# Optimization experiments

Measured on AMD Instinct MI355X. Metric: run time of the kernel, lower is better.

Reference implementation:

```python
import jax, jax.numpy as jnp
import numpy as np

# Representative causal-LM config (pre-LN GPT/Llama-style, eager attention)
L, D, H, FF, V = 2, 2048, 16, 8192, 32000
B, S = 2, 1024
DH = D // H
NEG = -1e9


def setup_inputs() -> dict:
    key = jax.random.key(0)
    ks = jax.random.split(key, 10)
    p = lambda k, shape: jax.random.normal(k, shape, dtype=jnp.float32) * 0.02
    return {
        "input_ids": jax.random.randint(ks[0], (B, S), 0, V),
        "attention_mask": jnp.ones((B, S), dtype=jnp.int32),
        "emb": p(ks[1], (V, D)),
        "ln1_g": jnp.ones((L, D)), "ln1_b": jnp.zeros((L, D)),
        "Wqkv": p(ks[2], (L, D, 3 * D)),
        "Wo": p(ks[3], (L, D, D)),
        "ln2_g": jnp.ones((L, D)), "ln2_b": jnp.zeros((L, D)),
        "W1": p(ks[4], (L, D, FF)), "W2": p(ks[5], (L, FF, D)),
        "lnf_g": jnp.ones((D,)), "lnf_b": jnp.zeros((D,)),
        "Wc1": p(ks[6], (D, D)), "bc1": jnp.zeros((D,)),
        "Wc2": p(ks[7], (D, 2)), "bc2": jnp.zeros((2,)),
    }


def _ln(x, g, b):
    m = x.mean(-1, keepdims=True)
    v = ((x - m) ** 2).mean(-1, keepdims=True)
    return (x - m) * jax.lax.rsqrt(v + 1e-5) * g + b


def _transformer_reward(input_ids, attention_mask, emb, ln1_g, ln1_b, Wqkv, Wo,
                        ln2_g, ln2_b, W1, W2, lnf_g, lnf_b, Wc1, bc1, Wc2, bc2):
    x = emb[input_ids]                                  # [B,S,D] embedding lookup
    causal = jnp.tril(jnp.ones((S, S), dtype=bool))     # [S,S]
    pad = attention_mask.astype(bool)[:, None, None, :] # [B,1,1,S]
    bias = jnp.where(causal[None, None] & pad, 0.0, NEG).astype(jnp.float32)
    scale = 1.0 / np.sqrt(DH).astype(np.float32)
    for l in range(L):
        h = _ln(x, ln1_g[l], ln1_b[l])
        qkv = h @ Wqkv[l]                               # [B,S,3D]
        q, k, v = jnp.split(qkv, 3, axis=-1)
        q = q.reshape(B, S, H, DH).transpose(0, 2, 1, 3)
        k = k.reshape(B, S, H, DH).transpose(0, 2, 1, 3)
        v = v.reshape(B, S, H, DH).transpose(0, 2, 1, 3)
        # eager attention: full [B,H,S,S] score matrix (as in attn_implementation='eager')
        scores = jnp.einsum('bhqd,bhkd->bhqk', q, k) * scale + bias
        attn = jax.nn.softmax(scores, axis=-1)
        o = jnp.einsum('bhqk,bhkd->bhqd', attn, v).transpose(0, 2, 1, 3).reshape(B, S, D)
        x = x + o @ Wo[l]
        h = _ln(x, ln2_g[l], ln2_b[l])
        x = x + jax.nn.gelu(h @ W1[l]) @ W2[l]
    hs = _ln(x, lnf_g, lnf_b)                           # hidden_states[-1]
    m = attention_mask[:, :, None].astype(jnp.float32)
    mean = (hs * m).sum(axis=1) / jnp.clip(m.sum(axis=1), 1e-9)  # masked mean pool
    logits = jnp.tanh(mean @ Wc1 + bc1) @ Wc2 + bc2     # classifier head
    return jax.nn.softmax(logits, axis=-1)[:, 1]        # rewards [B]


def reference(input_ids, attention_mask, emb, ln1_g, ln1_b, Wqkv, Wo,
              ln2_g, ln2_b, W1, W2, lnf_g, lnf_b, Wc1, bc1, Wc2, bc2):
    return _transformer_reward(input_ids, attention_mask, emb, ln1_g, ln1_b, Wqkv, Wo,
                               ln2_g, ln2_b, W1, W2, lnf_g, lnf_b, Wc1, bc1, Wc2, bc2)
```

## Files before the change

kernel.cpp:

```cpp
#include <hip/hip_runtime.h>
#include <hip/hip_bf16.h>

using bf16 = __hip_bfloat16;
typedef short s16x8 __attribute__((ext_vector_type(8)));
typedef float f32x4 __attribute__((ext_vector_type(4)));

static constexpr int D  = 2048;
static constexpr int H  = 16;
static constexpr int FF = 8192;
static constexpr int S  = 1024;
static constexpr int NB = 2;
static constexpr int DH = 128;
static constexpr int L  = 2;
static constexpr int BS = NB * S;
static constexpr int BH = NB * H;
static constexpr int D3 = 3 * D;

__device__ __forceinline__ float wave_sum(float v) {
#pragma unroll
  for (int o = 32; o > 0; o >>= 1) v += __shfl_down(v, o, 64);
  return v;
}
__device__ __forceinline__ float wave_max(float v) {
#pragma unroll
  for (int o = 32; o > 0; o >>= 1) v = fmaxf(v, __shfl_down(v, o, 64));
  return v;
}

__device__ __forceinline__ void gll16(const void* g, void* l) {
  __builtin_amdgcn_global_load_lds(
      (const __attribute__((address_space(1))) unsigned int*)g,
      (__attribute__((address_space(3))) unsigned int*)l, 16, 0, 0);
}

__device__ __forceinline__ float gelu_tanh(float x) {
  return 0.5f * x * (1.0f + tanhf(0.7978845608028654f * (x + 0.044715f * x * x * x)));
}

__device__ __forceinline__ void stv(float* p, long i, float v) { p[i] = v; }
__device__ __forceinline__ void stv(bf16* p, long i, float v)  { p[i] = __float2bfloat16(v); }

template <int EPI>
__launch_bounds__(256)
__global__ void gemm_k(const bf16* __restrict__ A, int lda, long sAb, long sAh,
                       const bf16* __restrict__ Bt, int ldb, long sBb, long sBh,
                       void* __restrict__ Cp, int ldc, long sCb, long sCh,
                       const float* __restrict__ resid, int K, int nH) {
  __shared__ __align__(16) bf16 lsA[2][128 * 32];
  __shared__ __align__(16) bf16 lsB[2][128 * 32];
  const int tid = threadIdx.x;
  const int zb = blockIdx.z / nH, zh = blockIdx.z % nH;
  const int m0 = blockIdx.y * 128, n0 = blockIdx.x * 128;
  const int sr = tid >> 2, sc = (tid & 3) * 8;
  const bf16* Ag = A + zb * sAb + zh * sAh + (long)(m0 + sr) * lda + sc;
  const bf16* Bg = Bt + zb * sBb + zh * sBh + (long)(n0 + sr) * ldb + sc;
  const long a64 = 64L * lda, b64 = 64L * ldb;

  const int lane = tid & 63, wv = tid >> 6;
  const int wm = (wv >> 1) * 64, wn = (wv & 1) * 64;
  const int fl = lane & 15, fg = lane >> 4;

  f32x4 acc[4][4];
#pragma unroll
  for (int i = 0; i < 4; i++)
#pragma unroll
    for (int j = 0; j < 4; j++) acc[i][j] = (f32x4){0.f, 0.f, 0.f, 0.f};

  gll16(Ag, lsA[0] + tid * 8);
  gll16(Ag + a64, lsA[0] + 2048 + tid * 8);
  gll16(Bg, lsB[0] + tid * 8);
  gll16(Bg + b64, lsB[0] + 2048 + tid * 8);
  __syncthreads();

  int it = 0;
  for (int k0 = 0; k0 < K; k0 += 32, it ^= 1) {
    const int nxt = it ^ 1;
    if (k0 + 32 < K) {
      gll16(Ag + k0 + 32, lsA[nxt] + tid * 8);
      gll16(Ag + a64 + k0 + 32, lsA[nxt] + 2048 + tid * 8);
      gll16(Bg + k0 + 32, lsB[nxt] + tid * 8);
      gll16(Bg + b64 + k0 + 32, lsB[nxt] + 2048 + tid * 8);
    }
    s16x8 af[4], bq[4];
#pragma unroll
    for (int i = 0; i < 4; i++) {
      af[i] = *(const s16x8*)(lsA[it] + (wm + i * 16 + fl) * 32 + fg * 8);
      bq[i] = *(const s16x8*)(lsB[it] + (wn + i * 16 + fl) * 32 + fg * 8);
    }
#pragma unroll
    for (int i = 0; i < 4; i++)
#pragma unroll
      for (int j = 0; j < 4; j++)
        acc[i][j] = __builtin_amdgcn_mfma_f32_16x16x32_bf16(af[i], bq[j], acc[i][j], 0, 0, 0);
    __syncthreads();
  }

  const long offC = zb * sCb + zh * sCh;
#pragma unroll
  for (int i = 0; i < 4; i++) {
#pragma unroll
    for (int j = 0; j < 4; j++) {
      const int row = m0 + wm + i * 16 + fg * 4;
      const int col = n0 + wn + j * 16 + fl;
#pragma unroll
      for (int r = 0; r < 4; r++) {
        const long ci = offC + (long)(row + r) * ldc + col;
        float v = acc[i][j][r];
        if (EPI == 0) {
          ((float*)Cp)[ci] = v;
        } else if (EPI == 1) {
          ((bf16*)Cp)[ci] = __float2bfloat16(v);
        } else if (EPI == 2) {
          ((float*)Cp)[ci] = v + resid[ci];
        } else {
          ((bf16*)Cp)[ci] = __float2bfloat16(gelu_tanh(v));
        }
      }
    }
  }
}

__launch_bounds__(256)
__global__ void reduce4_k(const float* __restrict__ p, float* __restrict__ x) {
  const long i = (long)blockIdx.x * 256 + threadIdx.x;
  const long n = (long)BS * D / 4;
  const float4 a = ((const float4*)p)[i];
  const float4 b = ((const float4*)p)[i + n];
  const float4 c = ((const float4*)p)[i + 2 * n];
  const float4 d2 = ((const float4*)p)[i + 3 * n];
  float4 xv = ((float4*)x)[i];
  xv.x += a.x + b.x + c.x + d2.x;
  xv.y += a.y + b.y + c.y + d2.y;
  xv.z += a.z + b.z + c.z + d2.z;
  xv.w += a.w + b.w + c.w + d2.w;
  ((float4*)x)[i] = xv;
}

__launch_bounds__(256)
__global__ void transcast_k(const float* __restrict__ in, bf16* __restrict__ out,
                            int R, int C) {
  __shared__ float tile[32][33];
  const int tx = threadIdx.x, ty = threadIdx.y;
  const int c0 = blockIdx.x * 32, r0 = blockIdx.y * 32;
#pragma unroll
  for (int k = 0; k < 4; k++)
    tile[ty + 8 * k][tx] = in[(long)(r0 + ty + 8 * k) * C + c0 + tx];
  __syncthreads();
#pragma unroll
  for (int k = 0; k < 4; k++)
    out[(long)(c0 + ty + 8 * k) * R + r0 + tx] = __float2bfloat16(tile[tx][ty + 8 * k]);
}

__launch_bounds__(256)
__global__ void vtrans_k(const bf16* __restrict__ qkv, bf16* __restrict__ Vt) {
  __shared__ bf16 tile[32][33];
  const int z = blockIdx.z, b = z / H, h = z % H;
  const int d0 = blockIdx.x * 32, s0 = blockIdx.y * 32;
  const int tx = threadIdx.x, ty = threadIdx.y;
#pragma unroll
  for (int k = 0; k < 4; k++)
    tile[ty + 8 * k][tx] =
        qkv[(long)(b * S + s0 + ty + 8 * k) * D3 + 2 * D + h * DH + d0 + tx];
  __syncthreads();
#pragma unroll
  for (int k = 0; k < 4; k++)
    Vt[((long)z * DH + d0 + ty + 8 * k) * S + s0 + tx] = tile[tx][ty + 8 * k];
}

template <typename OutT>
__launch_bounds__(256)
__global__ void ln_k(const float* __restrict__ x, const float* __restrict__ g,
                     const float* __restrict__ bb, OutT* __restrict__ out) {
  __shared__ float sA[4], sB[4];
  const long row = blockIdx.x;
  const int tid = threadIdx.x;
  const float4* xr = (const float4*)(x + row * D);
  float4 v0 = xr[tid], v1 = xr[tid + 256];
  float s = v0.x + v0.y + v0.z + v0.w + v1.x + v1.y + v1.z + v1.w;
  float ss = v0.x * v0.x + v0.y * v0.y + v0.z * v0.z + v0.w * v0.w +
             v1.x * v1.x + v1.y * v1.y + v1.z * v1.z + v1.w * v1.w;
  s = wave_sum(s);
  ss = wave_sum(ss);
  const int lane = tid & 63, wv = tid >> 6;
  if (lane == 0) { sA[wv] = s; sB[wv] = ss; }
  __syncthreads();
  s = sA[0] + sA[1] + sA[2] + sA[3];
  ss = sB[0] + sB[1] + sB[2] + sB[3];
  const float mean = s * (1.f / D);
  const float var = ss * (1.f / D) - mean * mean;
  const float rstd = rsqrtf(var + 1e-5f);
  const float4* gv = (const float4*)g;
  const float4* bv = (const float4*)bb;
  float4 g0 = gv[tid], g1 = gv[tid + 256], c0 = bv[tid], c1 = bv[tid + 256];
  OutT* orow = out + row * D;
  stv(orow, 4 * tid + 0, (v0.x - mean) * rstd * g0.x + c0.x);
  stv(orow, 4 * tid + 1, (v0.y - mean) * rstd * g0.y + c0.y);
  stv(orow, 4 * tid + 2, (v0.z - mean) * rstd * g0.z + c0.z);
  stv(orow, 4 * tid + 3, (v0.w - mean) * rstd * g0.w + c0.w);
  stv(orow, 1024 + 4 * tid + 0, (v1.x - mean) * rstd * g1.x + c1.x);
  stv(orow, 1024 + 4 * tid + 1, (v1.y - mean) * rstd * g1.y + c1.y);
  stv(orow, 1024 + 4 * tid + 2, (v1.z - mean) * rstd * g1.z + c1.z);
  stv(orow, 1024 + 4 * tid + 3, (v1.w - mean) * rstd * g1.w + c1.w);
}

__launch_bounds__(256)
__global__ void embed_k(const int* __restrict__ ids, const float* __restrict__ emb,
                        float* __restrict__ x) {
  const long gid = (long)blockIdx.x * 256 + threadIdx.x;
  const int tok = (int)(gid >> 9);
  const int c = (int)(gid & 511);
  const int id = ids[tok];
  ((float4*)x)[gid] = ((const float4*)(emb + (long)id * D))[c];
}

__launch_bounds__(256)
__global__ void softmax_k(float* __restrict__ scores, const int* __restrict__ amask,
                          float scale) {
  __shared__ float sred[4];
  const int q = blockIdx.x, z = blockIdx.y, b = z / H;
  float* row = scores + ((long)z * S + q) * S;
  const int tid = threadIdx.x;
  const int lane = tid & 63, wv = tid >> 6;
  float v[4];
  float mx = -3.4e38f;
#pragma unroll
  for (int i = 0; i < 4; i++) {
    const int k = tid + i * 256;
    const float s = row[k] * scale;
    const bool ok = (k <= q) && (amask[b * S + k] != 0);
    v[i] = s + (ok ? 0.f : -1e9f);
    mx = fmaxf(mx, v[i]);
  }
  mx = wave_max(mx);
  if (lane == 0) sred[wv] = mx;
  __syncthreads();
  mx = fmaxf(fmaxf(sred[0], sred[1]), fmaxf(sred[2], sred[3]));
  __syncthreads();
  float e[4], sm = 0.f;
#pragma unroll
  for (int i = 0; i < 4; i++) {
    e[i] = __expf(v[i] - mx);
    sm += e[i];
  }
  sm = wave_sum(sm);
  if (lane == 0) sred[wv] = sm;
  __syncthreads();
  sm = sred[0] + sred[1] + sred[2] + sred[3];
  const float inv = 1.f / sm;
  bf16* orow = (bf16*)row;
#pragma unroll
  for (int i = 0; i < 4; i++) orow[tid + i * 256] = __float2bfloat16(e[i] * inv);
}

__launch_bounds__(256)
__global__ void pool_k(const float* __restrict__ hs, const int* __restrict__ amask,
                       float* __restrict__ pooled) {
  const int d = blockIdx.x * 256 + threadIdx.x;
  const int b = blockIdx.y;
  float s = 0.f, cnt = 0.f;
  for (int i = 0; i < S; i++) {
    const float m = (float)amask[b * S + i];
    s += hs[((long)(b * S + i)) * D + d] * m;
    cnt += m;
  }
  pooled[b * D + d] = s / fmaxf(cnt, 1e-9f);
}

__launch_bounds__(256)
__global__ void head1_k(const float* __restrict__ pooled, const float* __restrict__ Wc1,
                        const float* __restrict__ bc1, float* __restrict__ t) {
  const int j = blockIdx.x * 256 + threadIdx.x;
  const int b = blockIdx.y;
  float s = bc1[j];
  for (int d = 0; d < D; d++) s += pooled[b * D + d] * Wc1[(long)d * D + j];
  t[b * D + j] = tanhf(s);
}

__launch_bounds__(256)
__global__ void head2_k(const float* __restrict__ t, const float* __restrict__ Wc2,
                        const float* __restrict__ bc2, float* __restrict__ out) {
  __shared__ float red[4][4];
  const int tid = threadIdx.x;
  const int lane = tid & 63, wv = tid >> 6;
  float a[4] = {0.f, 0.f, 0.f, 0.f};
  for (int j = tid; j < D; j += 256) {
    const float w0 = Wc2[j * 2 + 0], w1 = Wc2[j * 2 + 1];
    const float t0 = t[j], t1 = t[D + j];
    a[0] += t0 * w0; a[1] += t0 * w1; a[2] += t1 * w0; a[3] += t1 * w1;
  }
#pragma unroll
  for (int c = 0; c < 4; c++) a[c] = wave_sum(a[c]);
  if (lane == 0) {
#pragma unroll
    for (int c = 0; c < 4; c++) red[wv][c] = a[c];
  }
  __syncthreads();
  if (tid == 0) {
    float tot[4];
#pragma unroll
    for (int c = 0; c < 4; c++) tot[c] = red[0][c] + red[1][c] + red[2][c] + red[3][c];
    const float l00 = tot[0] + bc2[0], l01 = tot[1] + bc2[1];
    const float l10 = tot[2] + bc2[0], l11 = tot[3] + bc2[1];
    out[0] = 1.f / (1.f + __expf(l00 - l01));
    out[1] = 1.f / (1.f + __expf(l10 - l11));
  }
}

extern "C" void kernel_launch(void* const* d_in, const int* in_sizes, int n_in,
                              void* d_out, int out_size, void* d_ws, size_t ws_size,
                              hipStream_t stream) {
  (void)in_sizes; (void)n_in; (void)out_size; (void)ws_size;
  const int*   ids   = (const int*)d_in[0];
  const int*   amask = (const int*)d_in[1];
  const float* emb   = (const float*)d_in[2];
  const float* ln1g  = (const float*)d_in[3];
  const float* ln1b  = (const float*)d_in[4];
  const float* Wqkv  = (const float*)d_in[5];
  const float* Wo    = (const float*)d_in[6];
  const float* ln2g  = (const float*)d_in[7];
  const float* ln2b  = (const float*)d_in[8];
  const float* W1    = (const float*)d_in[9];
  const float* W2    = (const float*)d_in[10];
  const float* lnfg  = (const float*)d_in[11];
  const float* lnfb  = (const float*)d_in[12];
  const float* Wc1   = (const float*)d_in[13];
  const float* bc1   = (const float*)d_in[14];
  const float* Wc2   = (const float*)d_in[15];
  const float* bc2   = (const float*)d_in[16];
  float* out = (float*)d_out;

  char* ws = (char*)d_ws;
  size_t off = 0;
  auto alloc = [&](size_t bytes) {
    size_t r = off;
    off += (bytes + 255) & ~(size_t)255;
    return r;
  };
  bf16* Wqkv_t = (bf16*)(ws + alloc((size_t)D3 * D * 2));
  bf16* Wo_t   = (bf16*)(ws + alloc((size_t)D * D * 2));
  bf16* W1_t   = (bf16*)(ws + alloc((size_t)FF * D * 2));
  bf16* W2_t   = (bf16*)(ws + alloc((size_t)D * FF * 2));
  float* x     = (float*)(ws + alloc((size_t)BS * D * 4));
  bf16* h      = (bf16*)(ws + alloc((size_t)BS * D * 2));
  bf16* qkv    = (bf16*)(ws + alloc((size_t)BS * D3 * 2));
  bf16* Vt     = (bf16*)(ws + alloc((size_t)BH * DH * S * 2));
  bf16* o_buf  = (bf16*)(ws + alloc((size_t)BS * D * 2));
  float* pooled= (float*)(ws + alloc((size_t)NB * D * 4));
  float* tb    = (float*)(ws + alloc((size_t)NB * D * 4));
  char* big    = ws + alloc((size_t)BH * S * S * 4);
  float* scores = (float*)big;
  bf16*  ffb    = (bf16*)big;
  float* hs     = (float*)big;
  float* parts  = (float*)(big + ((size_t)BS * FF * 2 + 255 & ~(size_t)255));

  const float scale = 0.088388347648318447f;
  dim3 blk(256);
  dim3 tblk(32, 8);

  embed_k<<<4096, blk, 0, stream>>>(ids, emb, x);

  for (int l = 0; l < L; l++) {
    transcast_k<<<dim3(D3 / 32, D / 32), tblk, 0, stream>>>(Wqkv + (size_t)l * D * D3, Wqkv_t, D, D3);
    transcast_k<<<dim3(D / 32, D / 32), tblk, 0, stream>>>(Wo + (size_t)l * D * D, Wo_t, D, D);
    transcast_k<<<dim3(FF / 32, D / 32), tblk, 0, stream>>>(W1 + (size_t)l * D * FF, W1_t, D, FF);
    transcast_k<<<dim3(D / 32, FF / 32), tblk, 0, stream>>>(W2 + (size_t)l * FF * D, W2_t, FF, D);

    ln_k<bf16><<<BS, blk, 0, stream>>>(x, ln1g + (size_t)l * D, ln1b + (size_t)l * D, h);
    gemm_k<1><<<dim3(D3 / 128, BS / 128, 1), blk, 0, stream>>>(
        h, D, 0, 0, Wqkv_t, D, 0, 0, qkv, D3, 0, 0, nullptr, D, 1);
    vtrans_k<<<dim3(DH / 32, S / 32, BH), tblk, 0, stream>>>(qkv, Vt);
    gemm_k<0><<<dim3(S / 128, S / 128, BH), blk, 0, stream>>>(
        qkv, D3, (long)S * D3, DH,
        qkv + D, D3, (long)S * D3, DH,
        scores, S, (long)H * S * S, (long)S * S, nullptr, DH, H);
    softmax_k<<<dim3(S, BH), blk, 0, stream>>>(scores, amask, scale);
    gemm_k<1><<<dim3(DH / 128, S / 128, BH), blk, 0, stream>>>(
        (const bf16*)scores, 2 * S, (long)H * 2 * S * S, (long)2 * S * S,
        Vt, S, (long)H * DH * S, (long)DH * S,
        o_buf, D, (long)S * D, DH, nullptr, S, H);
    gemm_k<2><<<dim3(D / 128, BS / 128, 1), blk, 0, stream>>>(
        o_buf, D, 0, 0, Wo_t, D, 0, 0, x, D, 0, 0, x, D, 1);
    ln_k<bf16><<<BS, blk, 0, stream>>>(x, ln2g + (size_t)l * D, ln2b + (size_t)l * D, h);
    gemm_k<3><<<dim3(FF / 128, BS / 128, 1), blk, 0, stream>>>(
        h, D, 0, 0, W1_t, D, 0, 0, ffb, FF, 0, 0, nullptr, D, 1);
    gemm_k<0><<<dim3(D / 128, BS / 128, 4), blk, 0, stream>>>(
        ffb, FF, 0, 2048, W2_t, FF, 0, 2048,
        parts, D, 0, (long)BS * D, nullptr, 2048, 4);
    reduce4_k<<<dim3(BS * D / 4 / 256), blk, 0, stream>>>(parts, x);
  }

  ln_k<float><<<BS, blk, 0, stream>>>(x, lnfg, lnfb, hs);
  pool_k<<<dim3(D / 256, NB), blk, 0, stream>>>(hs, amask, pooled);
  head1_k<<<dim3(D / 256, NB), blk, 0, stream>>>(pooled, Wc1, bc1, tb);
  head2_k<<<1, blk, 0, stream>>>(tb, Wc2, bc2, out);
}
```

Before: 1.740 ms.

## Add 256x256-tile 8-wave pipelined GEMM for QKV, FFN1 and FFN2

Adds a new GEMM kernel that uses 256x256 output tiles with 512 threads. It double-buffers LDS via direct global-to-LDS loads, uses an XOR swizzle, and interleaves staging with MFMA phases under explicit waitcnt, barriers and setprio. The large projection GEMMs (QKV, W1 with GELU, split-K W2) now use it to raise arithmetic intensity and overlap loads with compute. Larger tiles give fewer blocks: the QKV launch has 24x8 blocks and W2 has 8x8x4, which may underfill the 256 CUs. The 128KB LDS per block also limits occupancy.

```diff
diff --git a/kernel.cpp b/kernel.cpp
--- a/kernel.cpp
+++ b/kernel.cpp
@@ -118,6 +118,174 @@
       }
     }
   }
+}
+
+template <int EPI>
+__launch_bounds__(512, 2)
+__global__ void gemm256_k(const bf16* __restrict__ A, int lda, long sAb, long sAh,
+                          const bf16* __restrict__ Bt, int ldb, long sBb, long sBh,
+                          void* __restrict__ Cp, int ldc, long sCb, long sCh,
+                          int K, int nH) {
+  __shared__ __align__(16) bf16 lsA[2][256 * 64];
+  __shared__ __align__(16) bf16 lsB[2][256 * 64];
+  const int tid = threadIdx.x;
+  const int zb = blockIdx.z / nH, zh = blockIdx.z % nH;
+  const int m0 = blockIdx.y * 256, n0 = blockIdx.x * 256;
+
+  const int sr = tid >> 3;
+  const int sc = (tid & 7) ^ (sr & 7);
+  const bf16* Ag = A + zb * sAb + zh * sAh + (long)(m0 + sr) * lda + sc * 8;
+  const bf16* Bg = Bt + zb * sBb + zh * sBh +
+                   (long)(n0 + (tid >> 8) * 64 + (sr & 31)) * ldb + sc * 8;
+
+  const int lane = tid & 63, wv = tid >> 6;
+  const int wm = wv >> 2;
+  const int wn = wv & 3;
+  const int fl = lane & 15, fg = lane >> 4;
+
+  const int aob = (wm * 64 + fl) * 64;
+  const int bob = (wn * 32 + fl) * 64;
+  const int s0 = ((fg) ^ (fl & 7)) * 8;
+  const int s1 = ((4 + fg) ^ (fl & 7)) * 8;
+
+  s16x8 a[4][2];
+  s16x8 bq[2][2][2];
+  f32x4 acc[2][4][2][2];
+#pragma unroll
+  for (int qm = 0; qm < 2; qm++)
+#pragma unroll
+    for (int mf = 0; mf < 4; mf++)
+#pragma unroll
+      for (int qn = 0; qn < 2; qn++)
+#pragma unroll
+        for (int nf = 0; nf < 2; nf++) acc[qm][mf][qn][nf] = (f32x4){0.f, 0.f, 0.f, 0.f};
+
+#define STAGE_A(buf, qm, kt)                                                  \
+  do {                                                                        \
+    const bf16* _s = Ag + (long)((qm) * 64) * lda + (kt) * 64;                \
+    gll16(_s, lsA[buf] + (qm) * 8192 + tid * 8);                              \
+    gll16(_s + 128L * lda, lsA[buf] + (qm) * 8192 + 4096 + tid * 8);          \
+  } while (0)
+#define STAGE_B(buf, qn, kt)                                                  \
+  do {                                                                        \
+    const bf16* _s = Bg + (long)((qn) * 32) * ldb + (kt) * 64;                \
+    gll16(_s, lsB[buf] + (qn) * 8192 + tid * 8);                              \
+    gll16(_s + 128L * ldb, lsB[buf] + (qn) * 8192 + 4096 + tid * 8);          \
+  } while (0)
+#define LDA8(buf, qm)                                                         \
+  do {                                                                        \
+    const bf16* _p = lsA[buf] + (qm) * 8192 + aob;                            \
+    a[0][0] = *(const s16x8*)(_p + s0);        a[0][1] = *(const s16x8*)(_p + s1);        \
+    a[1][0] = *(const s16x8*)(_p + 1024 + s0); a[1][1] = *(const s16x8*)(_p + 1024 + s1); \
+    a[2][0] = *(const s16x8*)(_p + 2048 + s0); a[2][1] = *(const s16x8*)(_p + 2048 + s1); \
+    a[3][0] = *(const s16x8*)(_p + 3072 + s0); a[3][1] = *(const s16x8*)(_p + 3072 + s1); \
+  } while (0)
+#define LDB4(buf, qn)                                                         \
+  do {                                                                        \
+    const bf16* _p = lsB[buf] + (qn) * 8192 + bob;                            \
+    bq[qn][0][0] = *(const s16x8*)(_p + s0);        bq[qn][0][1] = *(const s16x8*)(_p + s1);        \
+    bq[qn][1][0] = *(const s16x8*)(_p + 1024 + s0); bq[qn][1][1] = *(const s16x8*)(_p + 1024 + s1); \
+  } while (0)
+#define MM16(qm, qn)                                                          \
+  do {                                                                        \
+    _Pragma("unroll") for (int mf = 0; mf < 4; ++mf) {                        \
+      acc[qm][mf][qn][0] = __builtin_amdgcn_mfma_f32_16x16x32_bf16(           \
+          a[mf][0], bq[qn][0][0], acc[qm][mf][qn][0], 0, 0, 0);               \
+      acc[qm][mf][qn][1] = __builtin_amdgcn_mfma_f32_16x16x32_bf16(           \
+          a[mf][0], bq[qn][1][0], acc[qm][mf][qn][1], 0, 0, 0);               \
+      acc[qm][mf][qn][0] = __builtin_amdgcn_mfma_f32_16x16x32_bf16(           \
+          a[mf][1], bq[qn][0][1], acc[qm][mf][qn][0], 0, 0, 0);               \
+      acc[qm][mf][qn][1] = __builtin_amdgcn_mfma_f32_16x16x32_bf16(           \
+          a[mf][1], bq[qn][1][1], acc[qm][mf][qn][1], 0, 0, 0);               \
+    }                                                                         \
+  } while (0)
+#define PHASE_TAIL(qm, qn)                                                    \
+  __builtin_amdgcn_s_barrier();                                               \
+  asm volatile("s_waitcnt lgkmcnt(0)" ::: "memory");                          \
+  __builtin_amdgcn_sched_barrier(0);                                          \
+  __builtin_amdgcn_s_setprio(1);                                              \
+  MM16(qm, qn);                                                               \
+  __builtin_amdgcn_s_setprio(0);
+
+  const int NT = K >> 6;
+
+  STAGE_A(0, 0, 0); STAGE_B(0, 0, 0); STAGE_B(0, 1, 0); STAGE_A(0, 1, 0);
+  STAGE_A(1, 0, 1); STAGE_B(1, 0, 1); STAGE_B(1, 1, 1);
+  asm volatile("s_waitcnt vmcnt(6)" ::: "memory");
+  __builtin_amdgcn_s_barrier();
+
+  for (int t = 0; t < NT; t += 2) {
+    const bool nl = (t + 2 < NT);
+    LDA8(0, 0);
+    LDB4(0, 0);
+    STAGE_A(1, 1, t + 1);
+    PHASE_TAIL(0, 0);
+    __builtin_amdgcn_s_barrier();
+    LDB4(0, 1);
+    if (nl) STAGE_A(0, 0, t + 2);
+    PHASE_TAIL(0, 1);
+    __builtin_amdgcn_s_barrier();
+    LDA8(0, 1);
+    if (nl) STAGE_B(0, 0, t + 2);
+    PHASE_TAIL(1, 0);
+    __builtin_amdgcn_s_barrier();
+    if (nl) STAGE_B(0, 1, t + 2);
+    PHASE_TAIL(1, 1);
+    if (nl) asm volatile("s_waitcnt vmcnt(6)" ::: "memory");
+    else    asm volatile("s_waitcnt vmcnt(0)" ::: "memory");
+    __builtin_amdgcn_s_barrier();
+    LDA8(1, 0);
+    LDB4(1, 0);
+    if (nl) STAGE_A(0, 1, t + 2);
+    PHASE_TAIL(0, 0);
+    __builtin_amdgcn_s_barrier();
+    LDB4(1, 1);
+    if (nl) STAGE_A(1, 0, t + 3);
+    PHASE_TAIL(0, 1);
+    __builtin_amdgcn_s_barrier();
+    LDA8(1, 1);
+    if (nl) STAGE_B(1, 0, t + 3);
+    PHASE_TAIL(1, 0);
+    __builtin_amdgcn_s_barrier();
+    if (nl) STAGE_B(1, 1, t + 3);
+    PHASE_TAIL(1, 1);
+    if (nl) asm volatile("s_waitcnt vmcnt(6)" ::: "memory");
+    __builtin_amdgcn_s_barrier();
+  }
+
+  const long offC = zb * sCb + zh * sCh;
+#pragma unroll
+  for (int qm = 0; qm < 2; qm++) {
+#pragma unroll
+    for (int mf = 0; mf < 4; mf++) {
+#pragma unroll
+      for (int qn = 0; qn < 2; qn++) {
+#pragma unroll
+        for (int nf = 0; nf < 2; nf++) {
+          const int row = m0 + wm * 128 + qm * 64 + mf * 16 + fg * 4;
+          const int col = n0 + wn * 64 + qn * 32 + nf * 16 + fl;
+#pragma unroll
+          for (int r = 0; r < 4; r++) {
+            const long ci = offC + (long)(row + r) * ldc + col;
+            float v = acc[qm][mf][qn][nf][r];
+            if (EPI == 0) {
+              ((float*)Cp)[ci] = v;
+            } else if (EPI == 1) {
+              ((bf16*)Cp)[ci] = __float2bfloat16(v);
+            } else {
+              ((bf16*)Cp)[ci] = __float2bfloat16(gelu_tanh(v));
+            }
+          }
+        }
+      }
+    }
+  }
+#undef STAGE_A
+#undef STAGE_B
+#undef LDA8
+#undef LDB4
+#undef MM16
+#undef PHASE_TAIL
 }
 
 __launch_bounds__(256)
@@ -355,6 +523,7 @@
 
   const float scale = 0.088388347648318447f;
   dim3 blk(256);
+  dim3 blk5(512);
   dim3 tblk(32, 8);
 
   embed_k<<<4096, blk, 0, stream>>>(ids, emb, x);
@@ -366,8 +535,8 @@
     transcast_k<<<dim3(D / 32, FF / 32), tblk, 0, stream>>>(W2 + (size_t)l * FF * D, W2_t, FF, D);
 
     ln_k<bf16><<<BS, blk, 0, stream>>>(x, ln1g + (size_t)l * D, ln1b + (size_t)l * D, h);
-    gemm_k<1><<<dim3(D3 / 128, BS / 128, 1), blk, 0, stream>>>(
-        h, D, 0, 0, Wqkv_t, D, 0, 0, qkv, D3, 0, 0, nullptr, D, 1);
+    gemm256_k<1><<<dim3(D3 / 256, BS / 256, 1), blk5, 0, stream>>>(
+        h, D, 0, 0, Wqkv_t, D, 0, 0, qkv, D3, 0, 0, D, 1);
     vtrans_k<<<dim3(DH / 32, S / 32, BH), tblk, 0, stream>>>(qkv, Vt);
     gemm_k<0><<<dim3(S / 128, S / 128, BH), blk, 0, stream>>>(
         qkv, D3, (long)S * D3, DH,
@@ -381,11 +550,11 @@
     gemm_k<2><<<dim3(D / 128, BS / 128, 1), blk, 0, stream>>>(
         o_buf, D, 0, 0, Wo_t, D, 0, 0, x, D, 0, 0, x, D, 1);
     ln_k<bf16><<<BS, blk, 0, stream>>>(x, ln2g + (size_t)l * D, ln2b + (size_t)l * D, h);
-    gemm_k<3><<<dim3(FF / 128, BS / 128, 1), blk, 0, stream>>>(
-        h, D, 0, 0, W1_t, D, 0, 0, ffb, FF, 0, 0, nullptr, D, 1);
-    gemm_k<0><<<dim3(D / 128, BS / 128, 4), blk, 0, stream>>>(
+    gemm256_k<3><<<dim3(FF / 256, BS / 256, 1), blk5, 0, stream>>>(
+        h, D, 0, 0, W1_t, D, 0, 0, ffb, FF, 0, 0, D, 1);
+    gemm256_k<0><<<dim3(D / 256, BS / 256, 4), blk5, 0, stream>>>(
         ffb, FF, 0, 2048, W2_t, FF, 0, 2048,
-        parts, D, 0, (long)BS * D, nullptr, 2048, 4);
+        parts, D, 0, (long)BS * D, 2048, 4);
     reduce4_k<<<dim3(BS * D / 4 / 256), blk, 0, stream>>>(parts, x);
   }
 
```

Measured after the change: 1.660 ms. 1.05x faster.
